# Kernel tuning notes

Measured on AMD Instinct MI355X. Metric: run time of the kernel, lower is better.

## Reference

```python
import jax, jax.numpy as jnp
import numpy as np

N = 100000          # nodes
E = 1600000         # random edges (self loops appended in reference)
F_IN = 256          # dataset.num_features
NUM_CLASSES = 7     # dataset.num_classes
H = 2 * NUM_CLASSES # heads = 14
C = NUM_CLASSES     # per-head channels (concat=False)
NEG_SLOPE = 0.2     # GATConv default leaky_relu slope


def setup_inputs() -> dict:
    key = jax.random.key(0)
    ks = jax.random.split(key, 10)
    x = jax.random.normal(ks[0], (N, F_IN), jnp.float32)
    edge_index = jax.random.randint(ks[1], (2, E), 0, N, jnp.int32)
    def glorot(k, shape, fan_in):
        return jax.random.normal(k, shape, jnp.float32) * (1.0 / np.sqrt(fan_in))
    return {
        "x": x,
        "edge_index": edge_index,
        "W1": glorot(ks[2], (F_IN, H * C), F_IN),
        "a_src1": glorot(ks[3], (H, C), C),
        "a_dst1": glorot(ks[4], (H, C), C),
        "b1": jnp.zeros((C,), jnp.float32),
        "W2": glorot(ks[5], (C, H * C), C),
        "a_src2": glorot(ks[6], (H, C), C),
        "a_dst2": glorot(ks[7], (H, C), C),
        "b2": jnp.zeros((C,), jnp.float32),
    }


def gat_conv(x, src, dst, W, a_src, a_dst, b):
    # x: [N, Fin] -> per-head projections [N, H, C]
    xh = (x @ W).reshape(N, H, C)
    # per-node attention logits [N, H]
    al_src = jnp.einsum("nhc,hc->nh", xh, a_src)
    al_dst = jnp.einsum("nhc,hc->nh", xh, a_dst)
    # per-edge logits (message flows src -> dst)
    alpha = jax.nn.leaky_relu(al_src[src] + al_dst[dst], NEG_SLOPE)  # [E', H]
    # segment softmax over incoming edges of each destination node
    amax = jax.ops.segment_max(jax.lax.stop_gradient(alpha), dst, num_segments=N)
    alpha = jnp.exp(alpha - amax[dst])
    denom = jax.ops.segment_sum(alpha, dst, num_segments=N)
    alpha = alpha / denom[dst]
    # weighted messages, then MAX aggregation per destination (aggr='max')
    msg = alpha[:, :, None] * xh[src]                    # [E', H, C]
    out = jax.ops.segment_max(msg, dst, num_segments=N)  # [N, H, C]
    # concat=False -> mean over heads, plus bias
    return out.mean(axis=1) + b                          # [N, C]


def reference(x, edge_index, W1, a_src1, a_dst1, b1, W2, a_src2, a_dst2, b2):
    # GATConv(add_self_loops=True): append self loops so every node has >=1 in-edge
    loops = jnp.arange(N, dtype=edge_index.dtype)
    src = jnp.concatenate([edge_index[0], loops])
    dst = jnp.concatenate([edge_index[1], loops])
    h = gat_conv(x, src, dst, W1, a_src1, a_dst1, b1)
    h = jax.nn.relu(h)
    h = gat_conv(h, src, dst, W2, a_src2, a_dst2, b2)
    return jax.nn.log_softmax(h, axis=1)
```

## Files before the change

### kernel.cpp

```cpp
#include <hip/hip_runtime.h>
#include <math.h>

#define H  14
#define C  7
#define HC 98
#define FIN 256
#define NEG_SLOPE 0.2f
#define NPB 32
#define AGG_BLOCK (NPB * H)
#define LOG2E 1.44269504088896f

#define BSHIFT 9
#define BSIZE  512
#define NBUCK_MAX 256

typedef __attribute__((ext_vector_type(8))) short short8;
typedef __attribute__((ext_vector_type(4))) float floatx4;
typedef _Float16 h2 __attribute__((ext_vector_type(2)));

#define WT_ROWS   112
#define WT_STRIDE 264
#define XA_STRIDE 40
#define VS_STRIDE 99

__device__ __forceinline__ unsigned bf16r(float f) {
    unsigned u = __float_as_uint(f);
    return (u + 0x7FFFu + ((u >> 16) & 1u)) >> 16;
}

__device__ __forceinline__ h2 u2h(unsigned u) { return __builtin_bit_cast(h2, u); }
__device__ __forceinline__ unsigned hpk(float a, float b) {
    h2 v = { (_Float16)a, (_Float16)b };
    return __builtin_bit_cast(unsigned, v);
}
__device__ __forceinline__ float hhi(unsigned w) {
    unsigned short s = (unsigned short)(w >> 16);
    return (float)__builtin_bit_cast(_Float16, s);
}


__global__ void k_zero(int* __restrict__ p, int n) {
    int i = blockIdx.x * blockDim.x + threadIdx.x;
    if (i < n) p[i] = 0;
}

__global__ __launch_bounds__(256) void k_hist(const int* __restrict__ ei, int E,
                                              int* __restrict__ gcnt, int nb) {
    __shared__ int hist[NBUCK_MAX];
    const int t = threadIdx.x;
    for (int i = t; i < nb; i += 256) hist[i] = 0;
    __syncthreads();
    const int stride = gridDim.x * 256;
    for (int e = blockIdx.x * 256 + t; e < E; e += stride)
        atomicAdd(&hist[ei[E + e] >> BSHIFT], 1);
    __syncthreads();
    for (int i = t; i < nb; i += 256)
        if (hist[i]) atomicAdd(gcnt + i, hist[i]);
}

__global__ __launch_bounds__(1024) void k_bscan(const int* __restrict__ gcnt,
                                                int* __restrict__ boff, int* __restrict__ bcur,
                                                int* __restrict__ row_ptr, int nb, int N) {
    __shared__ int sd[1024];
    int t = threadIdx.x;
    int own = (t < nb) ? gcnt[t] : 0;
    sd[t] = own;
    __syncthreads();
    #pragma unroll
    for (int off = 1; off < 1024; off <<= 1) {
        int v = (t >= off) ? sd[t - off] : 0;
        __syncthreads();
        sd[t] += v;
        __syncthreads();
    }
    if (t < nb) {
        boff[t + 1] = sd[t];
        bcur[t] = sd[t] - own;
        if (t == nb - 1) row_ptr[N] = sd[t];
    }
    if (t == 0) boff[0] = 0;
}

__global__ __launch_bounds__(256) void k_part(const int* __restrict__ ei, int E,
                                              int* __restrict__ bcur, int2* __restrict__ pedge,
                                              int nb) {
    __shared__ int hist[NBUCK_MAX];
    __shared__ int start[NBUCK_MAX];
    const int t = threadIdx.x;
    const int chunk = (E + gridDim.x - 1) / gridDim.x;
    const int c0 = blockIdx.x * chunk;
    const int c1 = min(c0 + chunk, E);
    for (int i = t; i < nb; i += 256) hist[i] = 0;
    __syncthreads();
    for (int e = c0 + t; e < c1; e += 256)
        atomicAdd(&hist[ei[E + e] >> BSHIFT], 1);
    __syncthreads();
    for (int i = t; i < nb; i += 256) {
        int h = hist[i];
        start[i] = h ? atomicAdd(bcur + i, h) : 0;
        hist[i] = 0;
    }
    __syncthreads();
    for (int e = c0 + t; e < c1; e += 256) {
        int s = ei[e], d = ei[E + e];
        int b = d >> BSHIFT;
        int pos = start[b] + atomicAdd(&hist[b], 1);
        pedge[pos] = make_int2(s, d);
    }
}

__global__ __launch_bounds__(512) void k_bcsr(const int2* __restrict__ pedge,
                                              const int* __restrict__ boff,
                                              int* __restrict__ row_ptr, int* __restrict__ col,
                                              int N) {
    __shared__ int cnt[BSIZE];
    __shared__ int sc[BSIZE];
    __shared__ int cur[BSIZE];
    const int b  = blockIdx.x;
    const int t  = threadIdx.x;
    const int e0 = boff[b], e1 = boff[b + 1];
    const int base = b << BSHIFT;
    const int nv = min(BSIZE, N - base);
    cnt[t] = 0;
    __syncthreads();
    for (int e = e0 + t; e < e1; e += 512)
        atomicAdd(&cnt[pedge[e].y - base], 1);
    __syncthreads();
    sc[t] = cnt[t];
    __syncthreads();
    #pragma unroll
    for (int off = 1; off < BSIZE; off <<= 1) {
        int v = (t >= off) ? sc[t - off] : 0;
        __syncthreads();
        sc[t] += v;
        __syncthreads();
    }
    if (t < nv) {
        int excl = sc[t] - cnt[t];
        row_ptr[base + t] = e0 + excl;
        cur[t] = excl;
    }
    __syncthreads();
    for (int e = e0 + t; e < e1; e += 512) {
        int2 r = pedge[e];
        int d = r.y - base;
        int pos = e0 + atomicAdd(&cur[d], 1);
        col[pos] = r.x;
    }
}


__global__ void k_convW(const float* __restrict__ W, unsigned short* __restrict__ WtG) {
    int id = blockIdx.x * blockDim.x + threadIdx.x;
    int n = id >> 8, k = id & 255;
    float v = (n < HC) ? W[k * HC + n] : 0.f;
    WtG[id] = (unsigned short)(__float_as_uint(v) >> 16);
}

__global__ __launch_bounds__(256) void k_proj1_mfma(
    const float* __restrict__ x, const unsigned short* __restrict__ WtG,
    const float* __restrict__ asrc, const float* __restrict__ adst,
    uint4* __restrict__ xpack, float* __restrict__ aldst, int N)
{
    __shared__ unsigned short wt_s[WT_ROWS * WT_STRIDE];
    __shared__ unsigned short xa_s[64 * XA_STRIDE];
    __shared__ float as_s[HC], ad_s[HC];
    float* vals_s = (float*)wt_s;
    const int t  = threadIdx.x;
    const int wv = t >> 6;
    const int l  = t & 63;
    const int ln = l & 15;
    const int qd = l >> 4;
    const int rowBase = blockIdx.x * 64;

    #pragma unroll
    for (int i = 0; i < 14; ++i) {
        int f = i * 256 + t;
        int r = f >> 5, pos = f & 31;
        *(uint4*)(wt_s + r * WT_STRIDE + pos * 8) = ((const uint4*)WtG)[f];
    }
    if (t < HC) { as_s[t] = asrc[t]; ad_s[t] = adst[t]; }

    floatx4 acc[7] = {};

    for (int step = 0; step < 8; ++step) {
        const int k0 = step * 32;
        __syncthreads();
        #pragma unroll
        for (int i = 0; i < 2; ++i) {
            int idx = i * 256 + t;
            int r = idx >> 3, c4 = idx & 7;
            int gr = rowBase + r; if (gr >= N) gr = N - 1;
            float4 v = *(const float4*)(x + (size_t)gr * FIN + k0 + c4 * 4);
            ushort4 u;
            u.x = (unsigned short)(__float_as_uint(v.x) >> 16);
            u.y = (unsigned short)(__float_as_uint(v.y) >> 16);
            u.z = (unsigned short)(__float_as_uint(v.z) >> 16);
            u.w = (unsigned short)(__float_as_uint(v.w) >> 16);
            *(ushort4*)(xa_s + r * XA_STRIDE + c4 * 4) = u;
        }
        __syncthreads();
        short8 a = *(const short8*)(xa_s + ((wv << 4) + ln) * XA_STRIDE + qd * 8);
        #pragma unroll
        for (int ct = 0; ct < 7; ++ct) {
            short8 b = *(const short8*)(wt_s + (ct * 16 + ln) * WT_STRIDE + k0 + qd * 8);
            acc[ct] = __builtin_amdgcn_mfma_f32_16x16x32_bf16(a, b, acc[ct], 0, 0, 0);
        }
    }

    __syncthreads();
    #pragma unroll
    for (int ct = 0; ct < 7; ++ct) {
        int colg = ct * 16 + ln;
        if (colg < HC) {
            #pragma unroll
            for (int r = 0; r < 4; ++r)
                vals_s[((wv << 4) + (qd << 2) + r) * VS_STRIDE + colg] = acc[ct][r];
        }
    }
    __syncthreads();

    for (int p = t; p < 64 * H; p += 256) {
        int nl = p / H, h = p - nl * H;
        int gn = rowBase + nl;
        if (gn >= N) break;
        const float* vp = vals_s + nl * VS_STRIDE + h * C;
        float v[C];
        float s1 = 0.f, s2 = 0.f;
        #pragma unroll
        for (int c2 = 0; c2 < C; ++c2) {
            float f = vp[c2];
            v[c2] = f;
            s1 = fmaf(f, as_s[h * C + c2], s1);
            s2 = fmaf(f, ad_s[h * C + c2], s2);
        }
        uint4 pk;
        pk.x = hpk(v[0], v[1]);
        pk.y = hpk(v[2], v[3]);
        pk.z = hpk(v[4], v[5]);
        pk.w = hpk(v[6], s1 * LOG2E);
        xpack[(size_t)gn * H + h] = pk;
        aldst[(size_t)gn * H + h] = s2 * LOG2E;
    }
}


__global__ __launch_bounds__(256) void k_proj2_pack(
    const float* __restrict__ h1, const float* __restrict__ W,
    const float* __restrict__ asrc, const float* __restrict__ adst,
    uint4* __restrict__ xpack, float* __restrict__ aldst, int N)
{
    __shared__ float Ws[C * HC];
    __shared__ float as_s[HC], ad_s[HC];
    const int t = threadIdx.x;
    for (int i = t; i < C * HC; i += 256) Ws[i] = W[i];
    if (t < HC) { as_s[t] = asrc[t]; ad_s[t] = adst[t]; }
    __syncthreads();
    int n = blockIdx.x * 256 + t;
    if (n >= N) return;
    float xr[C];
    #pragma unroll
    for (int c2 = 0; c2 < C; ++c2) xr[c2] = h1[(size_t)n * C + c2];
    #pragma unroll
    for (int h = 0; h < H; ++h) {
        float v[C], s1 = 0.f, s2 = 0.f;
        #pragma unroll
        for (int c2 = 0; c2 < C; ++c2) {
            float acc = 0.f;
            #pragma unroll
            for (int k = 0; k < C; ++k)
                acc = fmaf(xr[k], Ws[k * HC + h * C + c2], acc);
            v[c2] = acc;
            s1 = fmaf(acc, as_s[h * C + c2], s1);
            s2 = fmaf(acc, ad_s[h * C + c2], s2);
        }
        uint4 pk;
        pk.x = hpk(v[0], v[1]);
        pk.y = hpk(v[2], v[3]);
        pk.z = hpk(v[4], v[5]);
        pk.w = hpk(v[6], s1 * LOG2E);
        xpack[(size_t)n * H + h] = pk;
        aldst[(size_t)n * H + h] = s2 * LOG2E;
    }
}

#define AGG_STEP(DEN, REC)                                              \
    {                                                                   \
        float l = hhi((REC).w) + ld;                                    \
        float p = __builtin_amdgcn_exp2f(fmaxf(l, 0.2f * l) - K);       \
        DEN += p;                                                       \
        _Float16 ph = (_Float16)p;                                      \
        h2 p2 = { ph, ph };                                             \
        m0 = __builtin_elementwise_max(m0, p2 * u2h((REC).x));          \
        m1 = __builtin_elementwise_max(m1, p2 * u2h((REC).y));          \
        m2 = __builtin_elementwise_max(m2, p2 * u2h((REC).z));          \
        m3 = __builtin_elementwise_max(m3, p2 * u2h((REC).w));          \
    }

template<int LAYER>
__global__ __launch_bounds__(AGG_BLOCK) void k_agg(
    const int* __restrict__ row_ptr, const int* __restrict__ col,
    const uint4* __restrict__ xpack, const float* __restrict__ aldst,
    const float* __restrict__ bias,
    float* __restrict__ h1, float* __restrict__ out, int N)
{
    __shared__ float vals[NPB][HC];
    __shared__ float fv[NPB][C];
    const int t  = threadIdx.x;
    const int nl = t / H;
    const int h  = t - nl * H;
    const int n  = blockIdx.x * NPB + nl;

    if (n < N) {
        const int e0  = row_ptr[n];
        const int deg = row_ptr[n + 1] - e0;
        const float ld = aldst[(size_t)n * H + h];
        const float kb = ld + 2.0f * LOG2E;
        const float K  = fmaxf(kb, 0.2f * kb);

        float denA, denB = 0.f;
        h2 m0, m1, m2, m3;
        {
            uint4 pk = xpack[(size_t)n * H + h];
            float l = hhi(pk.w) + ld;
            float p = __builtin_amdgcn_exp2f(fmaxf(l, 0.2f * l) - K);
            denA = p;
            _Float16 ph = (_Float16)p;
            h2 p2 = { ph, ph };
            m0 = p2 * u2h(pk.x);
            m1 = p2 * u2h(pk.y);
            m2 = p2 * u2h(pk.z);
            m3 = p2 * u2h(pk.w);
        }

        if (deg > 0) {
            const int last = deg - 1;
            int c0 = col[e0];
            int c1 = col[e0 + min(1, last)];
            int c2 = col[e0 + min(2, last)];
            int c3 = col[e0 + min(3, last)];
            uint4 r0 = xpack[(size_t)c0 * H + h];
            uint4 r1 = xpack[(size_t)c1 * H + h];
            uint4 r2 = xpack[(size_t)c2 * H + h];
            uint4 r3 = xpack[(size_t)c3 * H + h];
            c0 = col[e0 + min(4, last)];
            c1 = col[e0 + min(5, last)];
            c2 = col[e0 + min(6, last)];
            c3 = col[e0 + min(7, last)];
            for (int i = 0; i < deg; i += 2) {
                uint4 curA = r0, curB = r1;
                r0 = r2; r1 = r3;
                r2 = xpack[(size_t)c0 * H + h];
                r3 = xpack[(size_t)c1 * H + h];
                c0 = c2; c1 = c3;
                c2 = col[e0 + min(i + 8, last)];
                c3 = col[e0 + min(i + 9, last)];
                AGG_STEP(denA, curA);
                if (i + 1 < deg) AGG_STEP(denB, curB);
            }
        }

        float rd = 1.f / (denA + denB);
        float* vp = &vals[nl][h * C];
        vp[0] = (float)m0.x * rd; vp[1] = (float)m0.y * rd;
        vp[2] = (float)m1.x * rd; vp[3] = (float)m1.y * rd;
        vp[4] = (float)m2.x * rd; vp[5] = (float)m2.y * rd;
        vp[6] = (float)m3.x * rd;
    }
    __syncthreads();

    if (t < NPB * C) {
        int nl2 = t / C, c2 = t - nl2 * C;
        int n2 = blockIdx.x * NPB + nl2;
        if (n2 < N) {
            float s = 0.f;
            #pragma unroll
            for (int hh = 0; hh < H; ++hh) s += vals[nl2][hh * C + c2];
            float o = s * (1.f / H) + bias[c2];
            if (LAYER == 1) h1[(size_t)n2 * C + c2] = fmaxf(o, 0.f);
            else            fv[nl2][c2] = o;
        }
    }
    if (LAYER == 2) {
        __syncthreads();
        if (t < NPB) {
            int n2 = blockIdx.x * NPB + t;
            if (n2 < N) {
                float mv = -1e30f;
                #pragma unroll
                for (int c2 = 0; c2 < C; ++c2) mv = fmaxf(mv, fv[t][c2]);
                float lse = 0.f;
                #pragma unroll
                for (int c2 = 0; c2 < C; ++c2) lse += __expf(fv[t][c2] - mv);
                lse = logf(lse);
                #pragma unroll
                for (int c2 = 0; c2 < C; ++c2)
                    out[(size_t)n2 * C + c2] = fv[t][c2] - mv - lse;
            }
        }
    }
}


static inline size_t align16(size_t v) { return (v + 15) & ~(size_t)15; }

extern "C" void kernel_launch(void* const* d_in, const int* in_sizes, int n_in,
                              void* d_out, int out_size, void* d_ws, size_t ws_size,
                              hipStream_t stream)
{
    const float* x     = (const float*)d_in[0];
    const int*   ei    = (const int*)d_in[1];
    const float* W1    = (const float*)d_in[2];
    const float* asrc1 = (const float*)d_in[3];
    const float* adst1 = (const float*)d_in[4];
    const float* b1    = (const float*)d_in[5];
    const float* W2    = (const float*)d_in[6];
    const float* asrc2 = (const float*)d_in[7];
    const float* adst2 = (const float*)d_in[8];
    const float* b2    = (const float*)d_in[9];

    const int N  = in_sizes[0] / FIN;
    const int E  = in_sizes[1] / 2;
    const int nb = (N + BSIZE - 1) >> BSHIFT;

    char* w = (char*)d_ws;
    uint4* xpack   = (uint4*)w; w += align16((size_t)N * H * 16);
    int2*  pedge   = (int2*)w;  w += align16((size_t)E * 8);
    float* aldst   = (float*)w; w += align16((size_t)N * H * 4);
    float* h1      = (float*)w; w += align16((size_t)N * C * 4);
    int*   row_ptr = (int*)w;   w += align16((size_t)(N + 1) * 4);
    int*   col     = (int*)w;   w += align16((size_t)E * 4);
    int*   gcnt    = (int*)w;   w += align16((size_t)nb * 4);
    int*   boff    = (int*)w;   w += align16((size_t)(nb + 1) * 4);
    int*   bcur    = (int*)w;   w += align16((size_t)nb * 4);
    unsigned short* WtG = (unsigned short*)w; w += align16((size_t)WT_ROWS * FIN * 2);

    const int gAgg  = (N + NPB - 1) / NPB;
    const int gMfma = (N + 63) / 64;
    const int g256N = (N + 255) / 256;

    k_zero<<<1, 256, 0, stream>>>(gcnt, nb);
    k_hist<<<256, 256, 0, stream>>>(ei, E, gcnt, nb);
    k_bscan<<<1, 1024, 0, stream>>>(gcnt, boff, bcur, row_ptr, nb, N);
    k_part<<<256, 256, 0, stream>>>(ei, E, bcur, pedge, nb);
    k_bcsr<<<nb, 512, 0, stream>>>(pedge, boff, row_ptr, col, N);

    k_convW<<<(WT_ROWS * FIN + 255) / 256, 256, 0, stream>>>(W1, WtG);
    k_proj1_mfma<<<gMfma, 256, 0, stream>>>(x, WtG, asrc1, adst1, xpack, aldst, N);
    k_agg<1><<<gAgg, AGG_BLOCK, 0, stream>>>(row_ptr, col, xpack, aldst, b1,
                                             h1, (float*)d_out, N);
    k_proj2_pack<<<g256N, 256, 0, stream>>>(h1, W2, asrc2, adst2, xpack, aldst, N);
    k_agg<2><<<gAgg, AGG_BLOCK, 0, stream>>>(row_ptr, col, xpack, aldst, b2,
                                             h1, (float*)d_out, N);
}
```

Baseline: 412.3 us.

## Split each node's edges across four lane groups with wave-shuffle reductions

The aggregation kernel now gives each node a full 64-lane wavefront: 16 lanes per head slot (14 used) times 4 edge-groups, each group walking every 4th incoming edge. Partial softmax denominators and per-channel max messages are combined with xor shuffles across the groups. The head mean and the log-softmax are also done with shuffles instead of shared memory and __syncthreads. This targets the latency of long serial per-thread edge loops on high-degree nodes, at the cost of 2 of 16 lanes idle per group and extra shuffle work.

```diff
diff --git a/kernel.cpp b/kernel.cpp
--- a/kernel.cpp
+++ b/kernel.cpp
@@ -6,8 +6,6 @@
 #define HC 98
 #define FIN 256
 #define NEG_SLOPE 0.2f
-#define NPB 32
-#define AGG_BLOCK (NPB * H)
 #define LOG2E 1.44269504088896f
 
 #define BSHIFT 9
@@ -36,6 +34,11 @@
 __device__ __forceinline__ float hhi(unsigned w) {
     unsigned short s = (unsigned short)(w >> 16);
     return (float)__builtin_bit_cast(_Float16, s);
+}
+__device__ __forceinline__ h2 hshfl_max(h2 v, int mask) {
+    int u = __builtin_bit_cast(int, v);
+    int o = __shfl_xor(u, mask, 64);
+    return __builtin_elementwise_max(v, u2h((unsigned)o));
 }
 
 
@@ -298,33 +301,35 @@
     }
 
 template<int LAYER>
-__global__ __launch_bounds__(AGG_BLOCK) void k_agg(
+__global__ __launch_bounds__(256) void k_agg(
     const int* __restrict__ row_ptr, const int* __restrict__ col,
     const uint4* __restrict__ xpack, const float* __restrict__ aldst,
     const float* __restrict__ bias,
     float* __restrict__ h1, float* __restrict__ out, int N)
 {
-    __shared__ float vals[NPB][HC];
-    __shared__ float fv[NPB][C];
-    const int t  = threadIdx.x;
-    const int nl = t / H;
-    const int h  = t - nl * H;
-    const int n  = blockIdx.x * NPB + nl;
-
-    if (n < N) {
+    const int t    = threadIdx.x;
+    const int lane = t & 63;
+    const int e4   = lane >> 4;
+    const int h    = lane & 15;
+    const int n    = blockIdx.x * 4 + (t >> 6);
+    const bool act = (h < H) && (n < N);
+
+    float den = 0.f, den2 = 0.f;
+    h2 m0 = u2h(0xFC00FC00u), m1 = m0, m2 = m0, m3 = m0;
+    float ld = 0.f, K = 0.f;
+
+    if (act) {
         const int e0  = row_ptr[n];
         const int deg = row_ptr[n + 1] - e0;
-        const float ld = aldst[(size_t)n * H + h];
-        const float kb = ld + 2.0f * LOG2E;
-        const float K  = fmaxf(kb, 0.2f * kb);
-
-        float denA, denB = 0.f;
-        h2 m0, m1, m2, m3;
-        {
+        ld = aldst[(size_t)n * H + h];
+        float kb = ld + 2.0f * LOG2E;
+        K = fmaxf(kb, 0.2f * kb);
+
+        if (e4 == 0) {
             uint4 pk = xpack[(size_t)n * H + h];
             float l = hhi(pk.w) + ld;
             float p = __builtin_amdgcn_exp2f(fmaxf(l, 0.2f * l) - K);
-            denA = p;
+            den = p;
             _Float16 ph = (_Float16)p;
             h2 p2 = { ph, ph };
             m0 = p2 * u2h(pk.x);
@@ -335,68 +340,75 @@
 
         if (deg > 0) {
             const int last = deg - 1;
-            int c0 = col[e0];
-            int c1 = col[e0 + min(1, last)];
-            int c2 = col[e0 + min(2, last)];
-            int c3 = col[e0 + min(3, last)];
+            int i = e4;
+            int c0 = col[e0 + min(i,      last)];
+            int c1 = col[e0 + min(i + 4,  last)];
             uint4 r0 = xpack[(size_t)c0 * H + h];
             uint4 r1 = xpack[(size_t)c1 * H + h];
-            uint4 r2 = xpack[(size_t)c2 * H + h];
-            uint4 r3 = xpack[(size_t)c3 * H + h];
-            c0 = col[e0 + min(4, last)];
-            c1 = col[e0 + min(5, last)];
-            c2 = col[e0 + min(6, last)];
-            c3 = col[e0 + min(7, last)];
-            for (int i = 0; i < deg; i += 2) {
+            c0 = col[e0 + min(i + 8,  last)];
+            c1 = col[e0 + min(i + 12, last)];
+            for (; i < deg; i += 8) {
                 uint4 curA = r0, curB = r1;
-                r0 = r2; r1 = r3;
-                r2 = xpack[(size_t)c0 * H + h];
-                r3 = xpack[(size_t)c1 * H + h];
-                c0 = c2; c1 = c3;
-                c2 = col[e0 + min(i + 8, last)];
-                c3 = col[e0 + min(i + 9, last)];
-                AGG_STEP(denA, curA);
-                if (i + 1 < deg) AGG_STEP(denB, curB);
+                r0 = xpack[(size_t)c0 * H + h];
+                r1 = xpack[(size_t)c1 * H + h];
+                c0 = col[e0 + min(i + 16, last)];
+                c1 = col[e0 + min(i + 20, last)];
+                AGG_STEP(den,  curA);
+                if (i + 4 < deg) AGG_STEP(den2, curB);
             }
         }
-
-        float rd = 1.f / (denA + denB);
-        float* vp = &vals[nl][h * C];
-        vp[0] = (float)m0.x * rd; vp[1] = (float)m0.y * rd;
-        vp[2] = (float)m1.x * rd; vp[3] = (float)m1.y * rd;
-        vp[4] = (float)m2.x * rd; vp[5] = (float)m2.y * rd;
-        vp[6] = (float)m3.x * rd;
-    }
-    __syncthreads();
-
-    if (t < NPB * C) {
-        int nl2 = t / C, c2 = t - nl2 * C;
-        int n2 = blockIdx.x * NPB + nl2;
-        if (n2 < N) {
-            float s = 0.f;
+    }
+    den += den2;
+
+    den += __shfl_xor(den, 16, 64);
+    den += __shfl_xor(den, 32, 64);
+    m0 = hshfl_max(m0, 16); m0 = hshfl_max(m0, 32);
+    m1 = hshfl_max(m1, 16); m1 = hshfl_max(m1, 32);
+    m2 = hshfl_max(m2, 16); m2 = hshfl_max(m2, 32);
+    m3 = hshfl_max(m3, 16); m3 = hshfl_max(m3, 32);
+
+    float v[C];
+    if (act) {
+        float rd = 1.f / den;
+        v[0] = (float)m0.x * rd; v[1] = (float)m0.y * rd;
+        v[2] = (float)m1.x * rd; v[3] = (float)m1.y * rd;
+        v[4] = (float)m2.x * rd; v[5] = (float)m2.y * rd;
+        v[6] = (float)m3.x * rd;
+    } else {
+        #pragma unroll
+        for (int c = 0; c < C; ++c) v[c] = 0.f;
+    }
+
+    #pragma unroll
+    for (int off = 1; off <= 8; off <<= 1) {
+        #pragma unroll
+        for (int c = 0; c < C; ++c) v[c] += __shfl_xor(v[c], off, 64);
+    }
+
+    if (n >= N) return;
+    if (LAYER == 1) {
+        if (lane < C) {
+            float myv = v[0];
             #pragma unroll
-            for (int hh = 0; hh < H; ++hh) s += vals[nl2][hh * C + c2];
-            float o = s * (1.f / H) + bias[c2];
-            if (LAYER == 1) h1[(size_t)n2 * C + c2] = fmaxf(o, 0.f);
-            else            fv[nl2][c2] = o;
-        }
-    }
-    if (LAYER == 2) {
-        __syncthreads();
-        if (t < NPB) {
-            int n2 = blockIdx.x * NPB + t;
-            if (n2 < N) {
-                float mv = -1e30f;
-                #pragma unroll
-                for (int c2 = 0; c2 < C; ++c2) mv = fmaxf(mv, fv[t][c2]);
-                float lse = 0.f;
-                #pragma unroll
-                for (int c2 = 0; c2 < C; ++c2) lse += __expf(fv[t][c2] - mv);
-                lse = logf(lse);
-                #pragma unroll
-                for (int c2 = 0; c2 < C; ++c2)
-                    out[(size_t)n2 * C + c2] = fv[t][c2] - mv - lse;
-            }
+            for (int c = 1; c < C; ++c) if (lane == c) myv = v[c];
+            h1[(size_t)n * C + lane] = fmaxf(myv * (1.f / H) + bias[lane], 0.f);
+        }
+    } else {
+        float o[C];
+        #pragma unroll
+        for (int c = 0; c < C; ++c) o[c] = v[c] * (1.f / H) + bias[c];
+        float mv = o[0];
+        #pragma unroll
+        for (int c = 1; c < C; ++c) mv = fmaxf(mv, o[c]);
+        float lse = 0.f;
+        #pragma unroll
+        for (int c = 0; c < C; ++c) lse += __expf(o[c] - mv);
+        lse = logf(lse);
+        if (lane < C) {
+            float myo = o[0];
+            #pragma unroll
+            for (int c = 1; c < C; ++c) if (lane == c) myo = o[c];
+            out[(size_t)n * C + lane] = myo - mv - lse;
         }
     }
 }
@@ -435,7 +447,7 @@
     int*   bcur    = (int*)w;   w += align16((size_t)nb * 4);
     unsigned short* WtG = (unsigned short*)w; w += align16((size_t)WT_ROWS * FIN * 2);
 
-    const int gAgg  = (N + NPB - 1) / NPB;
+    const int gAgg  = (N + 3) / 4;
     const int gMfma = (N + 63) / 64;
     const int g256N = (N + 255) / 256;
 
@@ -447,9 +459,9 @@
 
     k_convW<<<(WT_ROWS * FIN + 255) / 256, 256, 0, stream>>>(W1, WtG);
     k_proj1_mfma<<<gMfma, 256, 0, stream>>>(x, WtG, asrc1, adst1, xpack, aldst, N);
-    k_agg<1><<<gAgg, AGG_BLOCK, 0, stream>>>(row_ptr, col, xpack, aldst, b1,
-                                             h1, (float*)d_out, N);
+    k_agg<1><<<gAgg, 256, 0, stream>>>(row_ptr, col, xpack, aldst, b1,
+                                       h1, (float*)d_out, N);
     k_proj2_pack<<<g256N, 256, 0, stream>>>(h1, W2, asrc2, adst2, xpack, aldst, N);
-    k_agg<2><<<gAgg, AGG_BLOCK, 0, stream>>>(row_ptr, col, xpack, aldst, b2,
-                                             h1, (float*)d_out, N);
-}
+    k_agg<2><<<gAgg, 256, 0, stream>>>(row_ptr, col, xpack, aldst, b2,
+                                       h1, (float*)d_out, N);
+}
```

Measured after the change: 409.8 us. No clear change (-0.6%).
